# Optimization experiments

Hardware: AMD Instinct MI355X
Metric: run time of the kernel (lower is better)

## Reference

```python
import jax, jax.numpy as jnp
import numpy as np


def setup_inputs() -> dict:
    key = jax.random.key(0)
    ks = jax.random.split(key, 5)
    B, S, C, H = 32, 512, 320, 512
    scale = 1.0 / np.sqrt(H)
    return {
        "x": jax.random.normal(ks[0], (B, S, C), dtype=jnp.float32),
        "w_ih": jax.random.normal(ks[1], (4 * H, S), dtype=jnp.float32) * scale,
        "w_hh": jax.random.normal(ks[2], (4 * H, H), dtype=jnp.float32) * scale,
        "b_ih": jax.random.normal(ks[3], (4 * H,), dtype=jnp.float32) * scale,
        "b_hh": jax.random.normal(ks[4], (4 * H,), dtype=jnp.float32) * scale,
    }


def reference(x, w_ih, w_hh, b_ih, b_hh):
    # x: (B, S, C). Original permutes to (B, C, S) and runs a length-1 LSTM per
    # channel with zero initial state -> single LSTM cell step:
    #   gates = x_c @ W_ih^T + b_ih + b_hh   (W_hh @ h0 == 0)
    # PyTorch gate order: i, f, g, o.
    B, S, C = x.shape
    H = w_hh.shape[1]
    gates = jnp.einsum("bsc,gs->bcg", x, w_ih) + b_ih + b_hh  # (B, C, 4H)
    i_g, f_g, g_g, o_g = jnp.split(gates, 4, axis=-1)
    c = jax.nn.sigmoid(i_g) * jnp.tanh(g_g)           # c0 = 0
    h = jax.nn.sigmoid(o_g) * jnp.tanh(c)             # (B, C, H)
    # Faithful to torch: cat over channels along batch dim -> (C*B, H),
    # then reshape to (B, C, H) (scrambles batch/channel order).
    h = jnp.transpose(h, (1, 0, 2)).reshape(B, C, H)
    # dropout is identity in eval mode
    return jnp.transpose(h, (0, 2, 1))                # (B, H, C)
```

## Files before the change

kernel.cpp:

```cpp
#include <hip/hip_runtime.h>
#include <stdint.h>

#define B_  32
#define S_  512
#define C_  320
#define H_  512

typedef __attribute__((ext_vector_type(8))) short short8;
typedef __attribute__((ext_vector_type(4))) float f32x4;

__device__ __forceinline__ unsigned short f2bf(float x){
  unsigned u = __builtin_bit_cast(unsigned, x);
  u = u + 0x7FFFu + ((u >> 16) & 1u);
  return (unsigned short)(u >> 16);
}
__device__ __forceinline__ float bf2f(unsigned short h){
  unsigned u = ((unsigned)h) << 16;
  return __builtin_bit_cast(float, u);
}
__device__ __forceinline__ float sigf(float x){ return 1.0f/(1.0f + __expf(-x)); }
__device__ __forceinline__ float tanh_fast(float x){ return 2.0f/(1.0f + __expf(-2.0f*x)) - 1.0f; }

__device__ __forceinline__ void gload16(const void* g, void* l){
  __builtin_amdgcn_global_load_lds((const __attribute__((address_space(1))) void*)g,
                                   (__attribute__((address_space(3))) void*)l, 16, 0, 0);
}

__global__ __launch_bounds__(256) void k_cast_w(const float* __restrict__ w,
                                                unsigned short* __restrict__ wws){
  int idx = blockIdx.x*256 + threadIdx.x;
  float4 v = ((const float4*)w)[idx];
  uint2 p;
  p.x = (unsigned)f2bf(v.x) | ((unsigned)f2bf(v.y) << 16);
  p.y = (unsigned)f2bf(v.z) | ((unsigned)f2bf(v.w) << 16);
  ((uint2*)wws)[idx] = p;
}

__global__ __launch_bounds__(256) void k_cast_tx(const float* __restrict__ x,
                                                 unsigned short* __restrict__ xws){
  __shared__ float lds[64][65];
  const int tid = threadIdx.x;
  const int st = blockIdx.x, ctt = blockIdx.y, b = blockIdx.z;
  const int s0 = st*64, c0 = ctt*64;
  const int row = tid >> 2, q = tid & 3;

  const float* src = x + ((size_t)(b*S_ + s0 + row))*C_ + c0 + q*16;
  #pragma unroll
  for (int j = 0; j < 4; j++){
    float4 v = ((const float4*)src)[j];
    lds[row][q*16 + j*4 + 0] = v.x;
    lds[row][q*16 + j*4 + 1] = v.y;
    lds[row][q*16 + j*4 + 2] = v.z;
    lds[row][q*16 + j*4 + 3] = v.w;
  }
  __syncthreads();
  const int crow = row;
  #pragma unroll
  for (int j = 0; j < 2; j++){
    short8 o;
    #pragma unroll
    for (int e = 0; e < 8; e++)
      o[e] = (short)f2bf(lds[q*16 + j*8 + e][crow]);
    *(short8*)(xws + ((size_t)(b*C_ + c0 + crow))*S_ + s0 + q*16 + j*8) = o;
  }
}

__global__ __launch_bounds__(256) void k_gemm(const unsigned short* __restrict__ wws,
                                              const unsigned short* __restrict__ xws,
                                              const float* __restrict__ b_ih,
                                              const float* __restrict__ b_hh,
                                              unsigned short* __restrict__ hws){
  __shared__ alignas(16) unsigned short ldsA[3*64*64];
  __shared__ alignas(16) unsigned short ldsB[64*64];

  const int tid  = threadIdx.x;
  const int w    = tid >> 6;
  const int lane = tid & 63;
  const int kt = blockIdx.x, ct = blockIdx.y, b = blockIdx.z;
  const int k0 = kt*64, c0 = ct*64;

  f32x4 acc[3][4];
  #pragma unroll
  for (int gi = 0; gi < 3; gi++)
    #pragma unroll
    for (int nf = 0; nf < 4; nf++)
      acc[gi][nf] = (f32x4){0.f, 0.f, 0.f, 0.f};

  const int cr   = lane >> 3;
  const int slot = ((lane & 7) ^ cr) << 4;

  for (int s0 = 0; s0 < S_; s0 += 64){
    #pragma unroll
    for (int i = 0; i < 8; i++){
      int q = w*8 + i;
      if (q < 24){
        int gi = q >> 3, q8 = q & 7;
        int gr = (gi == 0 ? 0 : (gi == 1 ? 1024 : 1536));
        int grow = gr + k0 + q8*8 + cr;
        const char* src = (const char*)wws + ((size_t)grow*S_ + s0)*2 + slot;
        char* dst = (char*)ldsA + gi*8192 + q8*1024;
        gload16(src, dst);
      } else {
        int q8 = q - 24;
        int xrow = b*C_ + c0 + q8*8 + cr;
        const char* src = (const char*)xws + ((size_t)xrow*S_ + s0)*2 + slot;
        char* dst = (char*)ldsB + q8*1024;
        gload16(src, dst);
      }
    }
    __syncthreads();

    #pragma unroll
    for (int ks = 0; ks < 2; ks++){
      const int colb = (ks*64 + ((lane >> 4) << 4)) ^ ((lane & 7) << 4);
      const int arow = w*16 + (lane & 15);
      short8 aF[3], bF[4];
      #pragma unroll
      for (int gi = 0; gi < 3; gi++)
        aF[gi] = *(const short8*)((const char*)ldsA + gi*8192 + arow*128 + colb);
      #pragma unroll
      for (int nf = 0; nf < 4; nf++){
        int brow = nf*16 + (lane & 15);
        bF[nf] = *(const short8*)((const char*)ldsB + brow*128 + colb);
      }
      #pragma unroll
      for (int gi = 0; gi < 3; gi++)
        #pragma unroll
        for (int nf = 0; nf < 4; nf++)
          acc[gi][nf] = __builtin_amdgcn_mfma_f32_16x16x32_bf16(aF[gi], bF[nf], acc[gi][nf], 0, 0, 0);
    }
    __syncthreads();
  }

  const int lkb = k0 + w*16 + ((lane >> 4) << 2);
  float bi[4], bg[4], bo[4];
  #pragma unroll
  for (int r = 0; r < 4; r++){
    bi[r] = b_ih[lkb + r]        + b_hh[lkb + r];
    bg[r] = b_ih[1024 + lkb + r] + b_hh[1024 + lkb + r];
    bo[r] = b_ih[1536 + lkb + r] + b_hh[1536 + lkb + r];
  }
  #pragma unroll
  for (int nf = 0; nf < 4; nf++){
    int c = c0 + nf*16 + (lane & 15);
    size_t n = (size_t)c*32 + (size_t)b;
    float h[4];
    #pragma unroll
    for (int r = 0; r < 4; r++){
      float iv = acc[0][nf][r] + bi[r];
      float gv = acc[1][nf][r] + bg[r];
      float ov = acc[2][nf][r] + bo[r];
      float cc = sigf(iv) * tanh_fast(gv);
      h[r] = sigf(ov) * tanh_fast(cc);
    }
    uint2 p;
    p.x = (unsigned)f2bf(h[0]) | ((unsigned)f2bf(h[1]) << 16);
    p.y = (unsigned)f2bf(h[2]) | ((unsigned)f2bf(h[3]) << 16);
    *(uint2*)(hws + n*H_ + lkb) = p;
  }
}

__global__ __launch_bounds__(256) void k_out(const unsigned short* __restrict__ hws,
                                             float* __restrict__ out){
  __shared__ float lds[64][65];
  const int tid = threadIdx.x;
  const int kt = blockIdx.x, ctt = blockIdx.y, b2 = blockIdx.z;
  const int k0 = kt*64, n0 = b2*320 + ctt*64;
  const int rr = tid >> 2, q = tid & 3;

  #pragma unroll
  for (int j = 0; j < 2; j++){
    short8 v = *(const short8*)(hws + ((size_t)(n0 + rr))*H_ + k0 + q*16 + j*8);
    #pragma unroll
    for (int e = 0; e < 8; e++)
      lds[rr][q*16 + j*8 + e] = bf2f((unsigned short)v[e]);
  }
  __syncthreads();
  const int krow = rr;
  #pragma unroll
  for (int j = 0; j < 4; j++){
    int c2l = q*16 + j*4;
    float4 o;
    o.x = lds[c2l + 0][krow];
    o.y = lds[c2l + 1][krow];
    o.z = lds[c2l + 2][krow];
    o.w = lds[c2l + 3][krow];
    *(float4*)(out + (size_t)b2*(H_*C_) + (size_t)(k0 + krow)*C_ + ctt*64 + c2l) = o;
  }
}

extern "C" void kernel_launch(void* const* d_in, const int* in_sizes, int n_in,
                              void* d_out, int out_size, void* d_ws, size_t ws_size,
                              hipStream_t stream){
  const float* x    = (const float*)d_in[0];
  const float* w_ih = (const float*)d_in[1];
  const float* b_ih = (const float*)d_in[3];
  const float* b_hh = (const float*)d_in[4];
  float* out = (float*)d_out;

  char* ws = (char*)d_ws;
  unsigned short* wws = (unsigned short*)(ws);
  unsigned short* xws = (unsigned short*)(ws + 2097152);
  unsigned short* hws = (unsigned short*)(ws + 2097152 + 10485760);

  k_cast_w <<<1024, 256, 0, stream>>>(w_ih, wws);
  k_cast_tx<<<dim3(8, 5, 32), 256, 0, stream>>>(x, xws);
  k_gemm   <<<dim3(8, 5, 32), 256, 0, stream>>>(wws, xws, b_ih, b_hh, hws);
  k_out    <<<dim3(8, 5, 32), 256, 0, stream>>>(hws, out);
}
```

Before: 65.07 us.

## Double-buffer LDS tiles in GEMM kernel to prefetch next K-slice

```diff
diff --git a/kernel.cpp b/kernel.cpp
--- a/kernel.cpp
+++ b/kernel.cpp
@@ -70,8 +70,7 @@
                                               const float* __restrict__ b_ih,
                                               const float* __restrict__ b_hh,
                                               unsigned short* __restrict__ hws){
-  __shared__ alignas(16) unsigned short ldsA[3*64*64];
-  __shared__ alignas(16) unsigned short ldsB[64*64];
+  __shared__ alignas(16) char lds[2][32768];
 
   const int tid  = threadIdx.x;
   const int w    = tid >> 6;
@@ -89,39 +88,54 @@
   const int cr   = lane >> 3;
   const int slot = ((lane & 7) ^ cr) << 4;
 
-  for (int s0 = 0; s0 < S_; s0 += 64){
-    #pragma unroll
-    for (int i = 0; i < 8; i++){
-      int q = w*8 + i;
-      if (q < 24){
-        int gi = q >> 3, q8 = q & 7;
-        int gr = (gi == 0 ? 0 : (gi == 1 ? 1024 : 1536));
-        int grow = gr + k0 + q8*8 + cr;
-        const char* src = (const char*)wws + ((size_t)grow*S_ + s0)*2 + slot;
-        char* dst = (char*)ldsA + gi*8192 + q8*1024;
-        gload16(src, dst);
-      } else {
-        int q8 = q - 24;
-        int xrow = b*C_ + c0 + q8*8 + cr;
-        const char* src = (const char*)xws + ((size_t)xrow*S_ + s0)*2 + slot;
-        char* dst = (char*)ldsB + q8*1024;
-        gload16(src, dst);
+  const char* srcp[8];
+  char*       dstp[8];
+  #pragma unroll
+  for (int i = 0; i < 8; i++){
+    int q = w*8 + i;
+    if (q < 24){
+      int gi = q >> 3, q8 = q & 7;
+      int gr = (gi == 0 ? 0 : (gi == 1 ? 1024 : 1536));
+      int grow = gr + k0 + q8*8 + cr;
+      srcp[i] = (const char*)wws + ((size_t)grow*S_)*2 + slot;
+      dstp[i] = &lds[0][0] + gi*8192 + q8*1024;
+    } else {
+      int q8 = q - 24;
+      int xrow = b*C_ + c0 + q8*8 + cr;
+      srcp[i] = (const char*)xws + ((size_t)xrow*S_)*2 + slot;
+      dstp[i] = &lds[0][0] + 24576 + q8*1024;
+    }
+  }
+
+  #pragma unroll
+  for (int i = 0; i < 8; i++){ gload16(srcp[i], dstp[i]); srcp[i] += 128; }
+  __syncthreads();
+
+  const int arow = w*16 + (lane & 15);
+  const int lo16 = (lane >> 4) << 4;
+  const int swz  = (lane & 7) << 4;
+
+  for (int t = 0; t < 8; t++){
+    const int p = t & 1;
+    if (t < 7){
+      #pragma unroll
+      for (int i = 0; i < 8; i++){
+        gload16(srcp[i], dstp[i] + (p^1)*32768);
+        srcp[i] += 128;
       }
     }
-    __syncthreads();
-
+    const char* base = &lds[p][0];
     #pragma unroll
     for (int ks = 0; ks < 2; ks++){
-      const int colb = (ks*64 + ((lane >> 4) << 4)) ^ ((lane & 7) << 4);
-      const int arow = w*16 + (lane & 15);
+      const int colb = (ks*64 + lo16) ^ swz;
       short8 aF[3], bF[4];
       #pragma unroll
       for (int gi = 0; gi < 3; gi++)
-        aF[gi] = *(const short8*)((const char*)ldsA + gi*8192 + arow*128 + colb);
+        aF[gi] = *(const short8*)(base + gi*8192 + arow*128 + colb);
       #pragma unroll
       for (int nf = 0; nf < 4; nf++){
         int brow = nf*16 + (lane & 15);
-        bF[nf] = *(const short8*)((const char*)ldsB + brow*128 + colb);
+        bF[nf] = *(const short8*)(base + 24576 + brow*128 + colb);
       }
       #pragma unroll
       for (int gi = 0; gi < 3; gi++)
@@ -153,10 +167,10 @@
       float cc = sigf(iv) * tanh_fast(gv);
       h[r] = sigf(ov) * tanh_fast(cc);
     }
-    uint2 p;
-    p.x = (unsigned)f2bf(h[0]) | ((unsigned)f2bf(h[1]) << 16);
-    p.y = (unsigned)f2bf(h[2]) | ((unsigned)f2bf(h[3]) << 16);
-    *(uint2*)(hws + n*H_ + lkb) = p;
+    uint2 p2;
+    p2.x = (unsigned)f2bf(h[0]) | ((unsigned)f2bf(h[1]) << 16);
+    p2.y = (unsigned)f2bf(h[2]) | ((unsigned)f2bf(h[3]) << 16);
+    *(uint2*)(hws + n*H_ + lkb) = p2;
   }
 }
 
```

Result: faster. 59.03 us (-9.3%).
